# Kernel tuning notes

Measured on AMD Instinct MI355X. Metric: run time of the kernel, lower is better.

The kernel has to match this reference:

```python
import jax, jax.numpy as jnp
import numpy as np
from jax import lax

BN_EPS = 1e-5

@jax.custom_vjp
def ste_sign(x):
    # Binarize to {-1, +1} (sign; 0 maps to 0 like torch.sign, negligible measure)
    return jnp.sign(x)

def _ste_fwd(x):
    return jnp.sign(x), x

def _ste_bwd(x, g):
    # Straight-through estimator: pass gradient where |x| <= 1
    return (g * (jnp.abs(x) <= 1.0).astype(g.dtype),)

ste_sign.defvjp(_ste_fwd, _ste_bwd)

def bin_conv3x3(x, w, stride=1):
    # Binarize both activations and weights, then 3x3 conv, padding=1, no bias
    xb = ste_sign(x)
    wb = ste_sign(w)
    return lax.conv_general_dilated(
        xb, wb, window_strides=(stride, stride), padding=((1, 1), (1, 1)),
        dimension_numbers=('NCHW', 'OIHW', 'NCHW'))

def batchnorm_inf(x, gamma, beta, mean, var):
    # Inference-mode BatchNorm2d over channel dim (axis=1)
    scale = gamma * lax.rsqrt(var + BN_EPS)
    shift = beta - mean * scale
    return x * scale[None, :, None, None] + shift[None, :, None, None]

def hardtanh(x):
    # SelfTanh modeled as hardtanh (standard BNN activation with STE-style grad)
    return jnp.clip(x, -1.0, 1.0)

def setup_inputs() -> dict:
    key = jax.random.key(0)
    ks = jax.random.split(key, 3)
    N, C, H, W = 64, 256, 56, 56
    x = jax.random.normal(ks[0], (N, C, H, W), dtype=jnp.float32)
    w1 = jax.random.normal(ks[1], (C, C, 3, 3), dtype=jnp.float32) * (1.0 / math_sqrt(9 * C))
    w2 = jax.random.normal(ks[2], (C, C, 3, 3), dtype=jnp.float32) * (1.0 / math_sqrt(9 * C))
    ones = jnp.ones((C,), jnp.float32)
    zeros = jnp.zeros((C,), jnp.float32)
    return {
        'x': x,
        'w1': w1, 'g1': ones, 'b1': zeros, 'm1': zeros, 'v1': ones,
        'w2': w2, 'g2': ones, 'b2': zeros, 'm2': zeros, 'v2': ones,
    }

def math_sqrt(v):
    return float(np.sqrt(v))

def reference(x, w1, g1, b1, m1, v1, w2, g2, b2, m2, v2):
    residual = x
    out = bin_conv3x3(x, w1, stride=1)
    out = batchnorm_inf(out, g1, b1, m1, v1)
    out = hardtanh(out)
    out = bin_conv3x3(out, w2, stride=1)
    out = batchnorm_inf(out, g2, b2, m2, v2)
    out = out + residual
    out = hardtanh(out)
    return out
```

## Files before the change

### kernel.cpp

```cpp
#include <hip/hip_runtime.h>
#include <stdint.h>


#define NB 64
#define C  256
#define H  56
#define W  56
#define HP 58
#define PPIX 272
#define SLOT (HP * PPIX)
#define OST 272

typedef int v4i __attribute__((ext_vector_type(4)));

__global__ __launch_bounds__(256)
void pack_x_kernel(const float* __restrict__ x, int8_t* __restrict__ Aq) {
    const int h = blockIdx.x, n = blockIdx.y;
    const int w  = threadIdx.x & 63;
    const int cq = threadIdx.x >> 6;

    __shared__ int8_t st[56 * OST];

    const float* xp = x + (((size_t)n * C + cq * 64) * H + h) * W + w;
#pragma unroll
    for (int i = 0; i < 16; ++i) {
        uint32_t u = 0;
#pragma unroll
        for (int b = 0; b < 4; ++b) {
            float v = (w < 56) ? xp[(size_t)(i * 4 + b) * (H * W)] : 0.0f;
            uint32_t t = (v < 0.0f) ? 0xFFu : ((v != 0.0f) ? 1u : 0u);
            u |= t << (8 * b);
        }
        if (w < 56)
            *(uint32_t*)(st + w * OST + cq * 64 + i * 4) = u;
    }
    __syncthreads();
    int8_t* dst = Aq + (((size_t)n * HP + h + 1) * HP + 1) * C;
    for (int idx = threadIdx.x; idx < 56 * 16; idx += 256) {
        int pix = idx >> 4, c16 = idx & 15;
        *(v4i*)(dst + (size_t)pix * C + c16 * 16) =
            *(const v4i*)(st + pix * OST + c16 * 16);
    }
}

__global__ __launch_bounds__(64)
void pack_w_kernel(const float* __restrict__ wa, const float* __restrict__ wb,
                   int8_t* __restrict__ B1, int8_t* __restrict__ B2) {
    const int kstep = blockIdx.x;
    const int nfrag = blockIdx.y;
    const float* wsrc = blockIdx.z ? wb : wa;
    int8_t* dst       = blockIdx.z ? B2 : B1;
    const int lane = threadIdx.x, quad = lane >> 4, l16 = lane & 15;
    const int co = nfrag * 16 + l16;
    uint32_t pk[4];
#pragma unroll
    for (int d = 0; d < 4; ++d) {
        uint32_t u = 0;
#pragma unroll
        for (int bb = 0; bb < 4; ++bb) {
            int k = kstep * 64 + quad * 16 + d * 4 + bb;
            int tap = k >> 8, ci = k & 255;
            float v = wsrc[((size_t)co * C + ci) * 9 + tap];
            uint32_t t = (v < 0.0f) ? 0xFFu : ((v != 0.0f) ? 1u : 0u);
            u |= t << (8 * bb);
        }
        pk[d] = u;
    }
    uint4 st; st.x = pk[0]; st.y = pk[1]; st.z = pk[2]; st.w = pk[3];
    *(uint4*)(dst + ((size_t)(nfrag * 36 + kstep) * 64 + lane) * 16) = st;
}

__global__ __launch_bounds__(256)
void halo_zero_kernel(int8_t* __restrict__ Aq, int8_t* __restrict__ Bq) {
    const int n = blockIdx.x;
    int8_t* buf = blockIdx.y ? Bq : Aq;
    const v4i z = (v4i){0, 0, 0, 0};
    for (int idx = threadIdx.x; idx < 228 * 16; idx += 256) {
        int px = idx >> 4, c16 = idx & 15;
        int row, col;
        if (px < 58)       { row = 0;  col = px; }
        else if (px < 116) { row = 57; col = px - 58; }
        else { int i = px - 116; row = 1 + (i >> 1); col = (i & 1) * 57; }
        *(v4i*)(buf + (((size_t)n * HP + row) * HP + col) * C + c16 * 16) = z;
    }
}

__global__ __launch_bounds__(256)
void bn_prep_kernel(const float* g1, const float* b1, const float* m1, const float* v1,
                    const float* g2, const float* b2, const float* m2, const float* v2,
                    float* __restrict__ sc, float* __restrict__ sh) {
    const int co = threadIdx.x;
    const float* g = blockIdx.x ? g2 : g1;
    const float* b = blockIdx.x ? b2 : b1;
    const float* m = blockIdx.x ? m2 : m1;
    const float* v = blockIdx.x ? v2 : v1;
    double scd = (double)g[co] / sqrt((double)v[co] + 1e-5);
    sc[blockIdx.x * C + co] = (float)scd;
    sh[blockIdx.x * C + co] = (float)((double)b[co] - (double)m[co] * scd);
}

template <int STAGE>
__global__ __launch_bounds__(256, 2)
void mconv_kernel(const int8_t* __restrict__ Aq, const int8_t* __restrict__ Bpk,
                  const float* __restrict__ scp, const float* __restrict__ shp,
                  const float* __restrict__ resid,
                  int8_t* __restrict__ Bout, float* __restrict__ out) {
    const int h2 = blockIdx.x;
    const int n  = blockIdx.y;
    const int tid = threadIdx.x;
    const int wv = tid >> 6, lane = tid & 63, quad = lane >> 4, l16 = lane & 15;

    __shared__ int8_t lds[4 * SLOT];

    const int8_t* gA = Aq + ((size_t)n * HP + h2 * 2) * HP * C;
    for (int idx = tid; idx < 4 * HP * 16; idx += 256) {
        int pix = idx >> 4, c16 = idx & 15;
        *(v4i*)(lds + pix * PPIX + c16 * 16) =
            *(const v4i*)(gA + (size_t)pix * C + c16 * 16);
    }
    __syncthreads();

    int abase[7];
#pragma unroll
    for (int f = 0; f < 7; ++f) {
        int mm = f * 16 + l16;
        int hl = (mm >= 56) ? 1 : 0;
        int w  = mm - 56 * hl;
        abase[f] = hl * SLOT + w * PPIX + quad * 16;
    }

    const int8_t* bq[4];
#pragma unroll
    for (int nf = 0; nf < 4; ++nf)
        bq[nf] = Bpk + (size_t)((wv * 4 + nf) * 36) * 1024 + lane * 16;

    v4i bcur[4];
#pragma unroll
    for (int nf = 0; nf < 4; ++nf) bcur[nf] = *(const v4i*)(bq[nf]);

    v4i acc[7][4];
#pragma unroll
    for (int f = 0; f < 7; ++f)
#pragma unroll
        for (int nf = 0; nf < 4; ++nf) acc[f][nf] = (v4i){0, 0, 0, 0};

#pragma unroll 1
    for (int t = 0; t < 9; ++t) {
        const int r = (t >= 6) ? 2 : ((t >= 3) ? 1 : 0);
        const int c = t - 3 * r;
        const int au = r * SLOT + c * PPIX;
#pragma unroll
        for (int ci = 0; ci < 4; ++ci) {
            v4i bnxt[4];
#pragma unroll
            for (int nf = 0; nf < 4; ++nf)
                bnxt[nf] = *(const v4i*)(bq[nf] + (ci + 1) * 1024);
            v4i afr[7];
#pragma unroll
            for (int f = 0; f < 7; ++f)
                afr[f] = *(const v4i*)(lds + abase[f] + au + ci * 64);
#pragma unroll
            for (int f = 0; f < 7; ++f)
#pragma unroll
                for (int nf = 0; nf < 4; ++nf)
                    acc[f][nf] = __builtin_amdgcn_mfma_i32_16x16x64_i8(
                        afr[f], bcur[nf], acc[f][nf], 0, 0, 0);
#pragma unroll
            for (int nf = 0; nf < 4; ++nf) bcur[nf] = bnxt[nf];
        }
#pragma unroll
        for (int nf = 0; nf < 4; ++nf) bq[nf] += 4096;
    }

    if (STAGE == 1) {
        __syncthreads();
#pragma unroll
        for (int nf = 0; nf < 4; ++nf) {
            const int co = (wv * 4 + nf) * 16 + l16;
            const float scale = scp[co], shift = shp[co];
#pragma unroll
            for (int f = 0; f < 7; ++f) {
#pragma unroll
                for (int reg = 0; reg < 4; ++reg) {
                    int mm = f * 16 + quad * 4 + reg;
                    float v = __fadd_rn(__fmul_rn((float)acc[f][nf][reg], scale), shift);
                    int8_t t8 = (v < 0.0f) ? (int8_t)-1
                              : ((v != 0.0f) ? (int8_t)1 : (int8_t)0);
                    lds[mm * OST + co] = t8;
                }
            }
        }
        __syncthreads();
        for (int idx = tid; idx < 112 * 16; idx += 256) {
            int mm = idx >> 4, c16 = idx & 15;
            int hl = (mm >= 56) ? 1 : 0;
            int ww = mm - 56 * hl;
            int oh = h2 * 2 + hl;
            *(v4i*)(Bout + (((size_t)n * HP + oh + 1) * HP + ww + 1) * C + c16 * 16)
                = *(const v4i*)(lds + mm * OST + c16 * 16);
        }
    } else {
#pragma unroll
        for (int nf = 0; nf < 4; ++nf) {
            const int co = (wv * 4 + nf) * 16 + l16;
            const float scale = scp[co], shift = shp[co];
#pragma unroll
            for (int f = 0; f < 7; ++f) {
                int mmb = f * 16 + quad * 4;
                int hl = (mmb >= 56) ? 1 : 0;
                int w0 = mmb - 56 * hl;
                int oh = h2 * 2 + hl;
                size_t ridx = (((size_t)n * C + co) * H + oh) * W + w0;
                float4 rv = *(const float4*)(resid + ridx);
                float rr[4] = {rv.x, rv.y, rv.z, rv.w};
                float oo[4];
#pragma unroll
                for (int reg = 0; reg < 4; ++reg) {
                    float v = __fadd_rn(__fmul_rn((float)acc[f][nf][reg], scale), shift);
                    float o = v + rr[reg];
                    oo[reg] = fminf(1.0f, fmaxf(-1.0f, o));
                }
                float4 ov; ov.x = oo[0]; ov.y = oo[1]; ov.z = oo[2]; ov.w = oo[3];
                *(float4*)(out + ridx) = ov;
            }
        }
    }
}

extern "C" void kernel_launch(void* const* d_in, const int* in_sizes, int n_in,
                              void* d_out, int out_size, void* d_ws, size_t ws_size,
                              hipStream_t stream) {
    const float* x  = (const float*)d_in[0];
    const float* w1 = (const float*)d_in[1];
    const float* g1 = (const float*)d_in[2];
    const float* b1 = (const float*)d_in[3];
    const float* m1 = (const float*)d_in[4];
    const float* v1 = (const float*)d_in[5];
    const float* w2 = (const float*)d_in[6];
    const float* g2 = (const float*)d_in[7];
    const float* b2 = (const float*)d_in[8];
    const float* m2 = (const float*)d_in[9];
    const float* v2 = (const float*)d_in[10];
    float* out = (float*)d_out;

    uint8_t* ws = (uint8_t*)d_ws;
    const size_t ASZ = (size_t)NB * HP * HP * C;
    const size_t WPK = (size_t)16 * 36 * 64 * 16;
    int8_t* Aq   = (int8_t*)(ws);
    int8_t* Bq   = (int8_t*)(ws + ASZ);
    int8_t* Bpk1 = (int8_t*)(ws + 2 * ASZ);
    int8_t* Bpk2 = (int8_t*)(ws + 2 * ASZ + WPK);
    float*  scb  = (float*)(ws + 2 * ASZ + 2 * WPK);
    float*  shb  = (float*)(ws + 2 * ASZ + 2 * WPK + 2048);

    halo_zero_kernel<<<dim3(NB, 2), 256, 0, stream>>>(Aq, Bq);
    bn_prep_kernel<<<dim3(2), 256, 0, stream>>>(g1, b1, m1, v1, g2, b2, m2, v2,
                                                scb, shb);
    pack_w_kernel<<<dim3(36, 16, 2), 64, 0, stream>>>(w1, w2, Bpk1, Bpk2);
    pack_x_kernel<<<dim3(H, NB), 256, 0, stream>>>(x, Aq);
    mconv_kernel<1><<<dim3(28, NB), 256, 0, stream>>>(Aq, Bpk1, scb, shb,
                                                      nullptr, Bq, nullptr);
    mconv_kernel<2><<<dim3(28, NB), 256, 0, stream>>>(Bq, Bpk2, scb + C, shb + C,
                                                      x, nullptr, out);
}
```

Baseline: 646.1 us.

## Fuse halo zeroing and BN prep into other kernels; double-buffer fully unrolled MFMA loop

Halo zeroing is folded into pack_x, which now covers padded rows, and the BN scale/shift computation moves into the conv epilogues, removing two kernel launches. The conv main loop is fully unrolled over all 36 k-steps. It double-buffers both LDS A fragments and global B fragments so the loads for the next step overlap the MFMAs of the current step. The trade-off is more VGPR pressure from the extra A buffers under launch_bounds(256,2), and redundant per-thread double-precision BN math in the epilogue.

```diff
diff --git a/kernel.cpp b/kernel.cpp
--- a/kernel.cpp
+++ b/kernel.cpp
@@ -14,14 +14,32 @@
 typedef int v4i __attribute__((ext_vector_type(4)));
 
 __global__ __launch_bounds__(256)
-void pack_x_kernel(const float* __restrict__ x, int8_t* __restrict__ Aq) {
-    const int h = blockIdx.x, n = blockIdx.y;
-    const int w  = threadIdx.x & 63;
-    const int cq = threadIdx.x >> 6;
-
+void pack_x_kernel(const float* __restrict__ x, int8_t* __restrict__ Aq,
+                   int8_t* __restrict__ Bq) {
+    const int hp = blockIdx.x;
+    const int n  = blockIdx.y;
+    const int tid = threadIdx.x;
+    int8_t* arow = Aq + ((size_t)n * HP + hp) * HP * C;
+    int8_t* brow = Bq + ((size_t)n * HP + hp) * HP * C;
+    const v4i z = (v4i){0, 0, 0, 0};
+
+    if (hp == 0 || hp == HP - 1) {
+        for (int idx = tid; idx < HP * 16; idx += 256) {
+            *(v4i*)(arow + (size_t)idx * 16) = z;
+            *(v4i*)(brow + (size_t)idx * 16) = z;
+        }
+        return;
+    }
+    if (tid < 64) {
+        int buf = tid >> 5, px = (tid >> 4) & 1, c16 = tid & 15;
+        int8_t* p = (buf ? brow : arow) + (size_t)(px ? (HP - 1) : 0) * C + c16 * 16;
+        *(v4i*)p = z;
+    }
+
+    const int w  = tid & 63;
+    const int cq = tid >> 6;
     __shared__ int8_t st[56 * OST];
-
-    const float* xp = x + (((size_t)n * C + cq * 64) * H + h) * W + w;
+    const float* xp = x + (((size_t)n * C + cq * 64) * H + (hp - 1)) * W + w;
 #pragma unroll
     for (int i = 0; i < 16; ++i) {
         uint32_t u = 0;
@@ -35,8 +53,8 @@
             *(uint32_t*)(st + w * OST + cq * 64 + i * 4) = u;
     }
     __syncthreads();
-    int8_t* dst = Aq + (((size_t)n * HP + h + 1) * HP + 1) * C;
-    for (int idx = threadIdx.x; idx < 56 * 16; idx += 256) {
+    int8_t* dst = arow + C;
+    for (int idx = tid; idx < 56 * 16; idx += 256) {
         int pix = idx >> 4, c16 = idx & 15;
         *(v4i*)(dst + (size_t)pix * C + c16 * 16) =
             *(const v4i*)(st + pix * OST + c16 * 16);
@@ -70,39 +88,11 @@
     *(uint4*)(dst + ((size_t)(nfrag * 36 + kstep) * 64 + lane) * 16) = st;
 }
 
-__global__ __launch_bounds__(256)
-void halo_zero_kernel(int8_t* __restrict__ Aq, int8_t* __restrict__ Bq) {
-    const int n = blockIdx.x;
-    int8_t* buf = blockIdx.y ? Bq : Aq;
-    const v4i z = (v4i){0, 0, 0, 0};
-    for (int idx = threadIdx.x; idx < 228 * 16; idx += 256) {
-        int px = idx >> 4, c16 = idx & 15;
-        int row, col;
-        if (px < 58)       { row = 0;  col = px; }
-        else if (px < 116) { row = 57; col = px - 58; }
-        else { int i = px - 116; row = 1 + (i >> 1); col = (i & 1) * 57; }
-        *(v4i*)(buf + (((size_t)n * HP + row) * HP + col) * C + c16 * 16) = z;
-    }
-}
-
-__global__ __launch_bounds__(256)
-void bn_prep_kernel(const float* g1, const float* b1, const float* m1, const float* v1,
-                    const float* g2, const float* b2, const float* m2, const float* v2,
-                    float* __restrict__ sc, float* __restrict__ sh) {
-    const int co = threadIdx.x;
-    const float* g = blockIdx.x ? g2 : g1;
-    const float* b = blockIdx.x ? b2 : b1;
-    const float* m = blockIdx.x ? m2 : m1;
-    const float* v = blockIdx.x ? v2 : v1;
-    double scd = (double)g[co] / sqrt((double)v[co] + 1e-5);
-    sc[blockIdx.x * C + co] = (float)scd;
-    sh[blockIdx.x * C + co] = (float)((double)b[co] - (double)m[co] * scd);
-}
-
 template <int STAGE>
 __global__ __launch_bounds__(256, 2)
 void mconv_kernel(const int8_t* __restrict__ Aq, const int8_t* __restrict__ Bpk,
-                  const float* __restrict__ scp, const float* __restrict__ shp,
+                  const float* __restrict__ gamma, const float* __restrict__ beta,
+                  const float* __restrict__ mean,  const float* __restrict__ var,
                   const float* __restrict__ resid,
                   int8_t* __restrict__ Bout, float* __restrict__ out) {
     const int h2 = blockIdx.x;
@@ -134,42 +124,40 @@
     for (int nf = 0; nf < 4; ++nf)
         bq[nf] = Bpk + (size_t)((wv * 4 + nf) * 36) * 1024 + lane * 16;
 
-    v4i bcur[4];
-#pragma unroll
-    for (int nf = 0; nf < 4; ++nf) bcur[nf] = *(const v4i*)(bq[nf]);
-
     v4i acc[7][4];
 #pragma unroll
     for (int f = 0; f < 7; ++f)
 #pragma unroll
         for (int nf = 0; nf < 4; ++nf) acc[f][nf] = (v4i){0, 0, 0, 0};
 
-#pragma unroll 1
-    for (int t = 0; t < 9; ++t) {
-        const int r = (t >= 6) ? 2 : ((t >= 3) ? 1 : 0);
-        const int c = t - 3 * r;
-        const int au = r * SLOT + c * PPIX;
-#pragma unroll
-        for (int ci = 0; ci < 4; ++ci) {
-            v4i bnxt[4];
+    v4i aA[7], aB[7], bA[4], bB[4];
+#pragma unroll
+    for (int f = 0; f < 7; ++f) aA[f] = *(const v4i*)(lds + abase[f]);
+#pragma unroll
+    for (int nf = 0; nf < 4; ++nf) bA[nf] = *(const v4i*)(bq[nf]);
+
+#pragma unroll
+    for (int u = 0; u < 36; ++u) {
+        const int un = u + 1;
+        const int tn = un >> 2, cin = un & 3;
+        const int rn = tn / 3, cn = tn - 3 * rn;
+        const int aun = (un < 36) ? (rn * SLOT + cn * PPIX + cin * 64) : 0;
+        v4i* ac  = (u & 1) ? aB : aA;
+        v4i* an  = (u & 1) ? aA : aB;
+        v4i* bc  = (u & 1) ? bB : bA;
+        v4i* bn_ = (u & 1) ? bA : bB;
+#pragma unroll
+        for (int f = 0; f < 7; ++f)
+            an[f] = *(const v4i*)(lds + abase[f] + aun);
+#pragma unroll
+        for (int nf = 0; nf < 4; ++nf)
+            bn_[nf] = *(const v4i*)(bq[nf] + (size_t)un * 1024);
+#pragma unroll
+        for (int f = 0; f < 7; ++f)
 #pragma unroll
             for (int nf = 0; nf < 4; ++nf)
-                bnxt[nf] = *(const v4i*)(bq[nf] + (ci + 1) * 1024);
-            v4i afr[7];
-#pragma unroll
-            for (int f = 0; f < 7; ++f)
-                afr[f] = *(const v4i*)(lds + abase[f] + au + ci * 64);
-#pragma unroll
-            for (int f = 0; f < 7; ++f)
-#pragma unroll
-                for (int nf = 0; nf < 4; ++nf)
-                    acc[f][nf] = __builtin_amdgcn_mfma_i32_16x16x64_i8(
-                        afr[f], bcur[nf], acc[f][nf], 0, 0, 0);
-#pragma unroll
-            for (int nf = 0; nf < 4; ++nf) bcur[nf] = bnxt[nf];
-        }
-#pragma unroll
-        for (int nf = 0; nf < 4; ++nf) bq[nf] += 4096;
+                acc[f][nf] = __builtin_amdgcn_mfma_i32_16x16x64_i8(
+                    ac[f], bc[nf], acc[f][nf], 0, 0, 0);
     }
 
     if (STAGE == 1) {
@@ -177,7 +165,9 @@
 #pragma unroll
         for (int nf = 0; nf < 4; ++nf) {
             const int co = (wv * 4 + nf) * 16 + l16;
-            const float scale = scp[co], shift = shp[co];
+            double scd = (double)gamma[co] / sqrt((double)var[co] + 1e-5);
+            float scale = (float)scd;
+            float shift = (float)((double)beta[co] - (double)mean[co] * scd);
 #pragma unroll
             for (int f = 0; f < 7; ++f) {
 #pragma unroll
@@ -203,7 +193,9 @@
 #pragma unroll
         for (int nf = 0; nf < 4; ++nf) {
             const int co = (wv * 4 + nf) * 16 + l16;
-            const float scale = scp[co], shift = shp[co];
+            double scd = (double)gamma[co] / sqrt((double)var[co] + 1e-5);
+            float scale = (float)scd;
+            float shift = (float)((double)beta[co] - (double)mean[co] * scd);
 #pragma unroll
             for (int f = 0; f < 7; ++f) {
                 int mmb = f * 16 + quad * 4;
@@ -250,16 +242,11 @@
     int8_t* Bq   = (int8_t*)(ws + ASZ);
     int8_t* Bpk1 = (int8_t*)(ws + 2 * ASZ);
     int8_t* Bpk2 = (int8_t*)(ws + 2 * ASZ + WPK);
-    float*  scb  = (float*)(ws + 2 * ASZ + 2 * WPK);
-    float*  shb  = (float*)(ws + 2 * ASZ + 2 * WPK + 2048);
-
-    halo_zero_kernel<<<dim3(NB, 2), 256, 0, stream>>>(Aq, Bq);
-    bn_prep_kernel<<<dim3(2), 256, 0, stream>>>(g1, b1, m1, v1, g2, b2, m2, v2,
-                                                scb, shb);
+
     pack_w_kernel<<<dim3(36, 16, 2), 64, 0, stream>>>(w1, w2, Bpk1, Bpk2);
-    pack_x_kernel<<<dim3(H, NB), 256, 0, stream>>>(x, Aq);
-    mconv_kernel<1><<<dim3(28, NB), 256, 0, stream>>>(Aq, Bpk1, scb, shb,
+    pack_x_kernel<<<dim3(HP, NB), 256, 0, stream>>>(x, Aq, Bq);
+    mconv_kernel<1><<<dim3(28, NB), 256, 0, stream>>>(Aq, Bpk1, g1, b1, m1, v1,
                                                       nullptr, Bq, nullptr);
-    mconv_kernel<2><<<dim3(28, NB), 256, 0, stream>>>(Bq, Bpk2, scb + C, shb + C,
+    mconv_kernel<2><<<dim3(28, NB), 256, 0, stream>>>(Bq, Bpk2, g2, b2, m2, v2,
                                                       x, nullptr, out);
 }
```

Result: slower. 692.1 us (+7.1%).
